# Performance work log

Measured on AMD Instinct MI355X. Metric: run time of the kernel, lower is better.

Reference implementation:

```python
import jax, jax.numpy as jnp
import numpy as np

# Llama-3.2-1B-style int4-quantized decoder (4 layers, reduced vocab)
L, D, H, HD, KVH, DFF, V, B, S = 4, 2048, 32, 64, 8, 8192, 32000, 4, 1024
ROPE_THETA = 500000.0


def setup_inputs() -> dict:
    key = jax.random.key(0)
    ks = jax.random.split(key, 18)
    def qw(k, shape):  # int4 weights stored in int32 carrier, range [-8, 8)
        return jax.random.randint(k, shape, -8, 8, dtype=jnp.int32)
    def sc(k, shape):  # per-output-channel dequant scales
        return jax.random.uniform(k, shape, jnp.float32, 0.005, 0.02)
    DKV = KVH * HD
    return {
        "token_ids": jax.random.randint(ks[0], (B, S), 0, V, dtype=jnp.int32),
        "embed": jax.random.normal(ks[1], (V, D), jnp.float32) * 0.02,
        "gamma_attn": jnp.ones((L, D), jnp.float32),
        "gamma_mlp": jnp.ones((L, D), jnp.float32),
        "gamma_final": jnp.ones((D,), jnp.float32),
        "wq": qw(ks[2], (L, D, D)),   "sq": sc(ks[3], (L, D)),
        "wk": qw(ks[4], (L, DKV, D)), "sk": sc(ks[5], (L, DKV)),
        "wv": qw(ks[6], (L, DKV, D)), "sv": sc(ks[7], (L, DKV)),
        "wo": qw(ks[8], (L, D, D)),   "so": sc(ks[9], (L, D)),
        "wg": qw(ks[10], (L, DFF, D)), "sg": sc(ks[11], (L, DFF)),
        "wu": qw(ks[12], (L, DFF, D)), "su": sc(ks[13], (L, DFF)),
        "wd": qw(ks[14], (L, D, DFF)), "sd": sc(ks[15], (L, D)),
    }


def _rmsnorm(x, g, eps=1e-5):
    return x * jax.lax.rsqrt(jnp.mean(x * x, axis=-1, keepdims=True) + eps) * g


def _rope(x):  # x: [B, S, n_heads, HD], split-half rotation (Llama convention)
    half = HD // 2
    inv_freq = ROPE_THETA ** (-jnp.arange(half, dtype=jnp.float32) * 2.0 / HD)
    ang = jnp.arange(x.shape[1], dtype=jnp.float32)[:, None] * inv_freq  # [S, half]
    cos = jnp.cos(ang)[None, :, None, :]
    sin = jnp.sin(ang)[None, :, None, :]
    x1, x2 = jnp.split(x, 2, axis=-1)
    return jnp.concatenate([x1 * cos - x2 * sin, x1 * sin + x2 * cos], axis=-1)


def _qlin(x, w_int, scale):
    # int4 dequant (per-out-channel symmetric) + matmul: y = x @ (w_int*scale)^T
    w = w_int.astype(jnp.float32) * scale[:, None]
    return jnp.einsum('bsd,od->bso', x, w)


def _forward(token_ids, embed, gamma_attn, gamma_mlp, gamma_final,
             wq, sq, wk, sk, wv, sv, wo, so, wg, sg, wu, su, wd, sd):
    x = embed[token_ids]                                    # [B, S, D]
    causal = jnp.tril(jnp.ones((S, S), dtype=bool))
    for l in range(L):
        # --- attention block ---
        h = _rmsnorm(x, gamma_attn[l])
        q = _qlin(h, wq[l], sq[l]).reshape(B, S, H, HD)
        k = _qlin(h, wk[l], sk[l]).reshape(B, S, KVH, HD)
        v = _qlin(h, wv[l], sv[l]).reshape(B, S, KVH, HD)
        q, k = _rope(q), _rope(k)
        k = jnp.repeat(k, H // KVH, axis=2)                 # GQA expand
        v = jnp.repeat(v, H // KVH, axis=2)
        scores = jnp.einsum('bqhd,bkhd->bhqk', q, k) / np.float32(np.sqrt(HD))
        scores = jnp.where(causal, scores, jnp.float32(-1e9))
        p = jax.nn.softmax(scores, axis=-1)
        attn = jnp.einsum('bhqk,bkhd->bqhd', p, v).reshape(B, S, D)
        x = x + _qlin(attn, wo[l], so[l])
        # --- SwiGLU MLP block ---
        h = _rmsnorm(x, gamma_mlp[l])
        g = jax.nn.silu(_qlin(h, wg[l], sg[l]))
        u = _qlin(h, wu[l], su[l])
        x = x + _qlin(g * u, wd[l], sd[l])
    x = _rmsnorm(x, gamma_final)
    # tied-embedding LM head; next-token logits at last position (decode step)
    return x[:, -1, :] @ embed.T                             # [B, V]


def reference(token_ids, embed, gamma_attn, gamma_mlp, gamma_final,
              wq, sq, wk, sk, wv, sv, wo, so, wg, sg, wu, su, wd, sd):
    return _forward(token_ids, embed, gamma_attn, gamma_mlp, gamma_final,
                    wq, sq, wk, sk, wv, sv, wo, so, wg, sg, wu, su, wd, sd)
```

## Files before the change

### kernel.cpp

```cpp
#include <hip/hip_runtime.h>
#include <hip/hip_bf16.h>

#define D_MODEL 2048
#define NH 32
#define HDIM 64
#define KVHEADS 8
#define DKV 512
#define DFF 8192
#define SEQ 1024
#define BATCH 4
#define NTOK 4096
#define VOCAB 32000
#define NLAYER 4

typedef __attribute__((ext_vector_type(8))) _Float16 f16x8;
typedef __attribute__((ext_vector_type(4))) _Float16 f16x4;
typedef __attribute__((ext_vector_type(4))) float f32x4;

static __device__ __forceinline__ void gload16(const void* g, void* l){
    __builtin_amdgcn_global_load_lds(
        (const __attribute__((address_space(1))) unsigned int*)g,
        (__attribute__((address_space(3))) unsigned int*)l, 16, 0, 0);
}

#define MFMA(d, x, y) d = __builtin_amdgcn_mfma_f32_16x16x32_f16(x, y, d, 0, 0, 0)
#define BAR()    __builtin_amdgcn_s_barrier()
#define LGK0()   do{ asm volatile("s_waitcnt lgkmcnt(0)" ::: "memory"); \
                     __builtin_amdgcn_sched_barrier(0); }while(0)
#define PRIO(x)  __builtin_amdgcn_s_setprio(x)

__global__ __launch_bounds__(256)
void gather_kernel(const int* __restrict__ tok, const float* __restrict__ embed,
                   float* __restrict__ X)
{
    int row = blockIdx.x;
    int id = tok[row];
    const float4* s = (const float4*)(embed + (size_t)id * D_MODEL);
    float4* d = (float4*)(X + (size_t)row * D_MODEL);
    d[threadIdx.x]       = s[threadIdx.x];
    d[threadIdx.x + 256] = s[threadIdx.x + 256];
}

__global__ __launch_bounds__(256)
void rope_table_kernel(float2* __restrict__ rt)
{
    int idx = blockIdx.x * 256 + threadIdx.x;
    int pos = idx >> 5, d = idx & 31;
    float inv = powf(500000.0f, -(float)d * (1.0f / 32.0f));
    float ang = (float)pos * inv;
    float s, c;
    sincosf(ang, &s, &c);
    rt[idx] = make_float2(c, s);
}

__global__ __launch_bounds__(256)
void wconv_all_kernel(const int* __restrict__ wq, const int* __restrict__ wk,
                      const int* __restrict__ wv, const int* __restrict__ wo,
                      const int* __restrict__ wg, const int* __restrict__ wu,
                      const int* __restrict__ wd, _Float16* __restrict__ O)
{
    int i = blockIdx.x * 256 + threadIdx.x;
    const int* s; int loc;
    if      (i <  1048576){ s = wq; loc = i; }
    else if (i <  1310720){ s = wk; loc = i - 1048576; }
    else if (i <  1572864){ s = wv; loc = i - 1310720; }
    else if (i <  2621440){ s = wo; loc = i - 1572864; }
    else if (i <  6815744){ s = wg; loc = i - 2621440; }
    else if (i < 11010048){ s = wu; loc = i - 6815744; }
    else                  { s = wd; loc = i - 11010048; }
    int4 w = ((const int4*)s)[loc];
    f16x4 o;
    o.x = (_Float16)(float)w.x; o.y = (_Float16)(float)w.y;
    o.z = (_Float16)(float)w.z; o.w = (_Float16)(float)w.w;
    ((f16x4*)O)[i] = o;
}

__global__ __launch_bounds__(256)
void rmsnorm_kernel(const float* __restrict__ X, const float* __restrict__ gamma,
                    _Float16* __restrict__ O)
{
    int row = blockIdx.x;
    const float* x = X + (size_t)row * D_MODEL;
    _Float16* o = O + (size_t)row * D_MODEL;
    int t = threadIdx.x;
    float4 v[2];
    float ss = 0.f;
#pragma unroll
    for (int i = 0; i < 2; i++){
        v[i] = *(const float4*)&x[(t + i*256)*4];
        ss += v[i].x*v[i].x + v[i].y*v[i].y + v[i].z*v[i].z + v[i].w*v[i].w;
    }
    for (int off = 32; off; off >>= 1) ss += __shfl_xor(ss, off, 64);
    __shared__ float red[4];
    __shared__ float invs;
    int lane = t & 63, wid = t >> 6;
    if (lane == 0) red[wid] = ss;
    __syncthreads();
    if (t == 0){
        float s = red[0] + red[1] + red[2] + red[3];
        invs = 1.0f / sqrtf(s / (float)D_MODEL + 1e-5f);
    }
    __syncthreads();
    float inv = invs;
#pragma unroll
    for (int i = 0; i < 2; i++){
        float4 g = *(const float4*)&gamma[(t + i*256)*4];
        f16x4 r;
        r.x = (_Float16)(v[i].x * inv * g.x); r.y = (_Float16)(v[i].y * inv * g.y);
        r.z = (_Float16)(v[i].z * inv * g.z); r.w = (_Float16)(v[i].w * inv * g.w);
        *(f16x4*)&o[(t + i*256)*4] = r;
    }
}

__global__ __launch_bounds__(256)
void final_norm_kernel(const float* __restrict__ X, const float* __restrict__ gamma,
                       float* __restrict__ XF)
{
    int b = blockIdx.x;
    const float* x = X + ((size_t)b * SEQ + SEQ - 1) * D_MODEL;
    float* o = XF + (size_t)b * D_MODEL;
    int t = threadIdx.x;
    float4 v[2];
    float ss = 0.f;
#pragma unroll
    for (int i = 0; i < 2; i++){
        v[i] = *(const float4*)&x[(t + i*256)*4];
        ss += v[i].x*v[i].x + v[i].y*v[i].y + v[i].z*v[i].z + v[i].w*v[i].w;
    }
    for (int off = 32; off; off >>= 1) ss += __shfl_xor(ss, off, 64);
    __shared__ float red[4];
    __shared__ float invs;
    int lane = t & 63, wid = t >> 6;
    if (lane == 0) red[wid] = ss;
    __syncthreads();
    if (t == 0){
        float s = red[0] + red[1] + red[2] + red[3];
        invs = 1.0f / sqrtf(s / (float)D_MODEL + 1e-5f);
    }
    __syncthreads();
    float inv = invs;
#pragma unroll
    for (int i = 0; i < 2; i++){
        float4 g = *(const float4*)&gamma[(t + i*256)*4];
        float4 r;
        r.x = v[i].x * inv * g.x; r.y = v[i].y * inv * g.y;
        r.z = v[i].z * inv * g.z; r.w = v[i].w * inv * g.w;
        *(float4*)&o[(t + i*256)*4] = r;
    }
}

__global__ __launch_bounds__(512, 2)
void gemm_mlp(const _Float16* __restrict__ A, const _Float16* __restrict__ WU,
              const _Float16* __restrict__ WG,
              const float* __restrict__ su, const float* __restrict__ sg,
              _Float16* __restrict__ U, int MT, int NT, int K)
{
    __shared__ __align__(16) _Float16 AS[2][256 * 64];
    __shared__ __align__(16) _Float16 US[2][128 * 64];
    __shared__ __align__(16) _Float16 GS[3][128 * 64];

    int nwg = MT * NT;
    int flat = blockIdx.x;
    int q = nwg >> 3, r = nwg & 7;
    int xcd = flat & 7, lid = flat >> 3;
    int swz = (xcd < r ? xcd * (q + 1) : r * (q + 1) + (xcd - r) * q) + lid;
    int bm = swz % MT, bn = swz / MT;
    int m0 = bm * 256, n0 = bn * 128;

    const int t = threadIdx.x;
    const int lane = t & 63, wid = t >> 6;
    const int ln15 = lane & 15, lq = lane >> 4;
    const int wm = wid >> 1, wn = wid & 1;
    const int sw = ln15 & 7;
    const int sl0 = (lq ^ sw) * 8, sl1 = ((4 + lq) ^ sw) * 8;

    const _Float16* srcA[4]; const _Float16* srcU[2]; const _Float16* srcG[2];
#pragma unroll
    for (int rr = 0; rr < 4; rr++){
        int ch = rr * 512 + t;
        int row = ch >> 3, s = (ch & 7) ^ (row & 7);
        srcA[rr] = A + (size_t)(m0 + row) * K + s * 8;
    }
#pragma unroll
    for (int rr = 0; rr < 2; rr++){
        int ch = rr * 512 + t;
        int row = ch >> 3, s = (ch & 7) ^ (row & 7);
        srcU[rr] = WU + (size_t)(n0 + row) * K + s * 8;
        srcG[rr] = WG + (size_t)(n0 + row) * K + s * 8;
    }
#define STG_A4(tile) do{ int _b = (tile) & 1; \
    gload16(srcA[0] + (size_t)(tile)*64, &AS[_b][(wid*64)*8]); \
    gload16(srcA[1] + (size_t)(tile)*64, &AS[_b][(512 + wid*64)*8]); \
    gload16(srcA[2] + (size_t)(tile)*64, &AS[_b][(1024 + wid*64)*8]); \
    gload16(srcA[3] + (size_t)(tile)*64, &AS[_b][(1536 + wid*64)*8]); }while(0)
#define STG_U2(tile) do{ int _b = (tile) & 1; \
    gload16(srcU[0] + (size_t)(tile)*64, &US[_b][(wid*64)*8]); \
    gload16(srcU[1] + (size_t)(tile)*64, &US[_b][(512 + wid*64)*8]); }while(0)
#define STG_G3(tile) do{ int _b = (tile) % 3; \
    gload16(srcG[0] + (size_t)(tile)*64, &GS[_b][(wid*64)*8]); \
    gload16(srcG[1] + (size_t)(tile)*64, &GS[_b][(512 + wid*64)*8]); }while(0)

    f32x4 accU[4][4], accG[4][4];
#pragma unroll
    for (int i = 0; i < 4; i++)
#pragma unroll
        for (int j = 0; j < 4; j++){
            accU[i][j] = (f32x4){0.f, 0.f, 0.f, 0.f};
            accG[i][j] = (f32x4){0.f, 0.f, 0.f, 0.f};
        }

    const int KT = K >> 6;

    STG_A4(0); STG_U2(0); STG_G3(0); STG_G3(1);
    asm volatile("s_waitcnt vmcnt(2)" ::: "memory");
    BAR();

    for (int kt = 0; kt < KT; ++kt){
        int cur = kt & 1, gcur = kt % 3;
        const _Float16* Ac = AS[cur];
        const _Float16* Uc = US[cur];
        const _Float16* Gc = GS[gcur];
        bool s1 = (kt + 1 < KT), s2 = (kt + 2 < KT);

        f16x8 afk0[4], afk1[4], buk0[4], buk1[4];
#pragma unroll
        for (int mf = 0; mf < 4; mf++)
            afk0[mf] = *(const f16x8*)&Ac[(wm * 64 + mf * 16 + ln15) * 64 + sl0];
#pragma unroll
        for (int nf = 0; nf < 4; nf++)
            buk0[nf] = *(const f16x8*)&Uc[(wn * 64 + nf * 16 + ln15) * 64 + sl0];
        if (s1) STG_A4(kt + 1);
        BAR(); LGK0(); PRIO(1);
#pragma unroll
        for (int mf = 0; mf < 4; mf++)
#pragma unroll
            for (int nf = 0; nf < 4; nf++)
                MFMA(accU[mf][nf], afk0[mf], buk0[nf]);
        PRIO(0); BAR();

#pragma unroll
        for (int mf = 0; mf < 4; mf++)
            afk1[mf] = *(const f16x8*)&Ac[(wm * 64 + mf * 16 + ln15) * 64 + sl1];
#pragma unroll
        for (int nf = 0; nf < 4; nf++)
            buk1[nf] = *(const f16x8*)&Uc[(wn * 64 + nf * 16 + ln15) * 64 + sl1];
        if (s1) STG_U2(kt + 1);
        BAR(); LGK0(); PRIO(1);
#pragma unroll
        for (int mf = 0; mf < 4; mf++)
#pragma unroll
            for (int nf = 0; nf < 4; nf++)
                MFMA(accU[mf][nf], afk1[mf], buk1[nf]);
        PRIO(0); BAR();

        f16x8 bgk0[4], bgk1[4];
#pragma unroll
        for (int nf = 0; nf < 4; nf++){
            bgk0[nf] = *(const f16x8*)&Gc[(wn * 64 + nf * 16 + ln15) * 64 + sl0];
            bgk1[nf] = *(const f16x8*)&Gc[(wn * 64 + nf * 16 + ln15) * 64 + sl1];
        }
        if (s2) STG_G3(kt + 2);
        BAR(); LGK0(); PRIO(1);
#pragma unroll
        for (int mf = 0; mf < 4; mf++)
#pragma unroll
            for (int nf = 0; nf < 4; nf++)
                MFMA(accG[mf][nf], afk0[mf], bgk0[nf]);
        PRIO(0); BAR();

        PRIO(1);
#pragma unroll
        for (int mf = 0; mf < 4; mf++)
#pragma unroll
            for (int nf = 0; nf < 4; nf++)
                MFMA(accG[mf][nf], afk1[mf], bgk1[nf]);
        PRIO(0);
        if (s1){
            if (s2) asm volatile("s_waitcnt vmcnt(2)" ::: "memory");
            else    asm volatile("s_waitcnt vmcnt(0)" ::: "memory");
            BAR();
            __builtin_amdgcn_sched_barrier(0);
        }
    }
#undef STG_A4
#undef STG_U2
#undef STG_G3

#pragma unroll
    for (int mf = 0; mf < 4; mf++){
        int rowb = m0 + wm * 64 + mf * 16 + lq * 4;
#pragma unroll
        for (int nf = 0; nf < 4; nf++){
            int colg = n0 + wn * 64 + nf * 16 + ln15;
            float scu = su[colg], scg = sg[colg];
#pragma unroll
            for (int rr2 = 0; rr2 < 4; rr2++){
                float uv = accU[mf][nf][rr2] * scu;
                float gv = accG[mf][nf][rr2] * scg;
                float sig = 1.0f / (1.0f + expf(-gv));
                U[(size_t)(rowb + rr2) * DFF + colg] = (_Float16)(gv * sig * uv);
            }
        }
    }
}

template<int EPI>
__global__ __launch_bounds__(512, 2)
void gemm_small(const _Float16* __restrict__ A, const _Float16* __restrict__ W,
                const float* __restrict__ sc0, const float* __restrict__ sc1,
                const float* __restrict__ sc2,
                void* __restrict__ C0, void* __restrict__ C1, void* __restrict__ C2,
                const float2* __restrict__ rt,
                int MT, int NT, int N, int K)
{
    __shared__ __align__(16) _Float16 AS[3][128 * 64];
    __shared__ __align__(16) _Float16 BS[3][256 * 64];

    int nwg = MT * NT;
    int flat = blockIdx.x;
    int q = nwg >> 3, r = nwg & 7;
    int xcd = flat & 7, lid = flat >> 3;
    int swz = (xcd < r ? xcd * (q + 1) : r * (q + 1) + (xcd - r) * q) + lid;
    int bm = swz % MT, bn = swz / MT;
    int m0 = bm * 128, n0 = bn * 256;

    const int t = threadIdx.x;
    const int lane = t & 63, wid = t >> 6;
    const int ln15 = lane & 15, lq = lane >> 4;
    const int wm = wid >> 2, wn = wid & 3;
    const int sw = ln15 & 7;
    const int sl0 = (lq ^ sw) * 8, sl1 = ((4 + lq) ^ sw) * 8;

    const _Float16* srcA[2]; const _Float16* srcB[4];
#pragma unroll
    for (int rr = 0; rr < 2; rr++){
        int ch = rr * 512 + t;
        int row = ch >> 3, s = (ch & 7) ^ (row & 7);
        srcA[rr] = A + (size_t)(m0 + row) * K + s * 8;
    }
#pragma unroll
    for (int rr = 0; rr < 4; rr++){
        int ch = rr * 512 + t;
        int row = ch >> 3, s = (ch & 7) ^ (row & 7);
        srcB[rr] = W + (size_t)(n0 + row) * K + s * 8;
    }
#define STG_A3(tile) do{ int _b = (tile) % 3; \
    gload16(srcA[0] + (size_t)(tile)*64, &AS[_b][(wid*64)*8]); \
    gload16(srcA[1] + (size_t)(tile)*64, &AS[_b][(512 + wid*64)*8]); }while(0)
#define STG_B3(tile) do{ int _b = (tile) % 3; \
    gload16(srcB[0] + (size_t)(tile)*64, &BS[_b][(wid*64)*8]); \
    gload16(srcB[1] + (size_t)(tile)*64, &BS[_b][(512 + wid*64)*8]); \
    gload16(srcB[2] + (size_t)(tile)*64, &BS[_b][(1024 + wid*64)*8]); \
    gload16(srcB[3] + (size_t)(tile)*64, &BS[_b][(1536 + wid*64)*8]); }while(0)

    f32x4 acc[4][4];
#pragma unroll
    for (int i = 0; i < 4; i++)
#pragma unroll
        for (int j = 0; j < 4; j++) acc[i][j] = (f32x4){0.f, 0.f, 0.f, 0.f};

    const int KT = K >> 6;

    STG_A3(0); STG_B3(0); STG_A3(1); STG_B3(1);
    asm volatile("s_waitcnt vmcnt(6)" ::: "memory");
    BAR();

    for (int kt = 0; kt < KT; ++kt){
        int cur = kt % 3;
        const _Float16* Ac = AS[cur];
        const _Float16* Bc = BS[cur];
        bool s1 = (kt + 1 < KT), s2 = (kt + 2 < KT);

        f16x8 af0[4], af1[4], bk0[4], bk1[4];
#pragma unroll
        for (int mf = 0; mf < 4; mf++)
            af0[mf] = *(const f16x8*)&Ac[(wm * 64 + mf * 16 + ln15) * 64 + sl0];
#pragma unroll
        for (int nf = 0; nf < 4; nf++)
            bk0[nf] = *(const f16x8*)&Bc[(wn * 64 + nf * 16 + ln15) * 64 + sl0];
        if (s2) STG_B3(kt + 2);
        BAR(); LGK0(); PRIO(1);
#pragma unroll
        for (int mf = 0; mf < 4; mf++)
#pragma unroll
            for (int nf = 0; nf < 4; nf++)
                MFMA(acc[mf][nf], af0[mf], bk0[nf]);
        PRIO(0); BAR();

#pragma unroll
        for (int mf = 0; mf < 4; mf++)
            af1[mf] = *(const f16x8*)&Ac[(wm * 64 + mf * 16 + ln15) * 64 + sl1];
#pragma unroll
        for (int nf = 0; nf < 4; nf++)
            bk1[nf] = *(const f16x8*)&Bc[(wn * 64 + nf * 16 + ln15) * 64 + sl1];
        if (s2) STG_A3(kt + 2);
        BAR(); LGK0(); PRIO(1);
#pragma unroll
        for (int mf = 0; mf < 4; mf++)
#pragma unroll
            for (int nf = 0; nf < 4; nf++)
                MFMA(acc[mf][nf], af1[mf], bk1[nf]);
        PRIO(0);
        if (s1){
            if (s2) asm volatile("s_waitcnt vmcnt(6)" ::: "memory");
            else    asm volatile("s_waitcnt vmcnt(0)" ::: "memory");
            BAR();
            __builtin_amdgcn_sched_barrier(0);
        }
    }
#undef STG_A3
#undef STG_B3

    if (EPI == 3){
        const float* sp; _Float16* dp; int nloc, nstr;
        if (n0 < 2048)      { sp = sc0; dp = (_Float16*)C0; nloc = n0;        nstr = 2048; }
        else if (n0 < 2560) { sp = sc1; dp = (_Float16*)C1; nloc = n0 - 2048; nstr = 512; }
        else                { sp = sc2; dp = (_Float16*)C2; nloc = n0 - 2560; nstr = 512; }
        bool dorope = (n0 < 2560);
        if (dorope){
#pragma unroll
            for (int mf = 0; mf < 4; mf++){
                int rowb = m0 + wm * 64 + mf * 16 + lq * 4;
#pragma unroll
                for (int nf = 0; nf < 2; nf++){
                    int colg = wn * 64 + nf * 16 + ln15;
                    int d = nf * 16 + ln15;
                    float s1v = sp[nloc + colg], s2v = sp[nloc + colg + 32];
#pragma unroll
                    for (int rr2 = 0; rr2 < 4; rr2++){
                        int row = rowb + rr2;
                        int pos = row & (SEQ - 1);
                        float2 cs = rt[pos * 32 + d];
                        float x1 = acc[mf][nf][rr2] * s1v;
                        float x2 = acc[mf][nf + 2][rr2] * s2v;
                        dp[(size_t)row * nstr + nloc + colg]      = (_Float16)(x1 * cs.x - x2 * cs.y);
                        dp[(size_t)row * nstr + nloc + colg + 32] = (_Float16)(x1 * cs.y + x2 * cs.x);
                    }
                }
            }
        } else {
#pragma unroll
            for (int mf = 0; mf < 4; mf++){
                int rowb = m0 + wm * 64 + mf * 16 + lq * 4;
#pragma unroll
                for (int nf = 0; nf < 4; nf++){
                    int colg = wn * 64 + nf * 16 + ln15;
                    float sc = sp[nloc + colg];
#pragma unroll
                    for (int rr2 = 0; rr2 < 4; rr2++)
                        dp[(size_t)(rowb + rr2) * nstr + nloc + colg] =
                            (_Float16)(acc[mf][nf][rr2] * sc);
                }
            }
        }
    } else {
#pragma unroll
        for (int mf = 0; mf < 4; mf++){
            int rowb = m0 + wm * 64 + mf * 16 + lq * 4;
#pragma unroll
            for (int nf = 0; nf < 4; nf++){
                int colg = n0 + wn * 64 + nf * 16 + ln15;
                float sc = sc0[colg];
#pragma unroll
                for (int rr2 = 0; rr2 < 4; rr2++){
                    size_t idx = (size_t)(rowb + rr2) * N + colg;
                    float val = acc[mf][nf][rr2] * sc;
                    if (EPI == 0){
                        ((_Float16*)C0)[idx] = (_Float16)val;
                    } else {
                        ((float*)C0)[idx] += val;
                    }
                }
            }
        }
    }
}

__global__ __launch_bounds__(256)
void attn_kernel(const _Float16* __restrict__ Qb, const _Float16* __restrict__ Kb,
                 const _Float16* __restrict__ Vb, _Float16* __restrict__ Ob)
{
    int bid = blockIdx.x;
    int qt = bid >> 7, h = bid & 31, b = (bid >> 5) & 3;
    int kvh = h >> 2;
    int q0 = qt * 128;
    int t = threadIdx.x, lane = t & 63, wid = t >> 6;
    int ln15 = lane & 15, lq = lane >> 4;

    __shared__ __align__(16) _Float16 Ksm[64 * 72];
    __shared__ __align__(16) _Float16 Vt[64 * 72];
    __shared__ __align__(16) _Float16 Pl[128 * 72];

    f16x8 qf[2][2];
    int qrow_g = b * SEQ + q0 + wid * 32;
#pragma unroll
    for (int mf = 0; mf < 2; mf++)
#pragma unroll
        for (int dc = 0; dc < 2; dc++)
            qf[mf][dc] = *(const f16x8*)(Qb + (size_t)(qrow_g + mf * 16 + ln15) * D_MODEL
                                         + h * HDIM + dc * 32 + lq * 8);

    f32x4 outv[2][4];
#pragma unroll
    for (int i = 0; i < 2; i++)
#pragma unroll
        for (int j = 0; j < 4; j++) outv[i][j] = (f32x4){0.f, 0.f, 0.f, 0.f};
    float mrun[2][4], lrun[2][4];
#pragma unroll
    for (int i = 0; i < 2; i++)
#pragma unroll
        for (int r = 0; r < 4; r++){ mrun[i][r] = -1e30f; lrun[i][r] = 0.f; }

    int ntile = (q0 + 128) >> 6;
    int ld_row = (t + 0) >> 3, ld_c8 = t & 7;
    int ld_row1 = (t + 256) >> 3;

    f16x8 k8[2], v8[2];
    {
        size_t base0 = (size_t)(b * SEQ + ld_row) * DKV + kvh * HDIM + ld_c8 * 8;
        size_t base1 = (size_t)(b * SEQ + ld_row1) * DKV + kvh * HDIM + ld_c8 * 8;
        k8[0] = *(const f16x8*)&Kb[base0];  v8[0] = *(const f16x8*)&Vb[base0];
        k8[1] = *(const f16x8*)&Kb[base1];  v8[1] = *(const f16x8*)&Vb[base1];
    }

    for (int kt = 0; kt < ntile; kt++){
        __syncthreads();
#pragma unroll
        for (int i = 0; i < 2; i++){
            int row = (i == 0) ? ld_row : ld_row1;
            *(f16x8*)&Ksm[row * 72 + ld_c8 * 8] = k8[i];
#pragma unroll
            for (int j = 0; j < 8; j++)
                Vt[(ld_c8 * 8 + j) * 72 + row] = v8[i][j];
        }
        __syncthreads();

        if (kt + 1 < ntile){
            size_t base0 = (size_t)(b * SEQ + (kt + 1) * 64 + ld_row) * DKV + kvh * HDIM + ld_c8 * 8;
            size_t base1 = (size_t)(b * SEQ + (kt + 1) * 64 + ld_row1) * DKV + kvh * HDIM + ld_c8 * 8;
            k8[0] = *(const f16x8*)&Kb[base0];  v8[0] = *(const f16x8*)&Vb[base0];
            k8[1] = *(const f16x8*)&Kb[base1];  v8[1] = *(const f16x8*)&Vb[base1];
        }

#pragma unroll
        for (int mf = 0; mf < 2; mf++){
            f32x4 sa[4];
#pragma unroll
            for (int kvf = 0; kvf < 4; kvf++) sa[kvf] = (f32x4){0.f, 0.f, 0.f, 0.f};
#pragma unroll
            for (int kvf = 0; kvf < 4; kvf++)
#pragma unroll
                for (int dc = 0; dc < 2; dc++){
                    f16x8 kb = *(const f16x8*)&Ksm[(kvf * 16 + ln15) * 72 + dc * 32 + lq * 8];
                    sa[kvf] = __builtin_amdgcn_mfma_f32_16x16x32_f16(qf[mf][dc], kb, sa[kvf], 0, 0, 0);
                }
            int qbase = q0 + wid * 32 + mf * 16 + lq * 4;
            float rowmax[4] = {-1e30f, -1e30f, -1e30f, -1e30f};
#pragma unroll
            for (int kvf = 0; kvf < 4; kvf++){
                int kva = kt * 64 + kvf * 16 + ln15;
#pragma unroll
                for (int r = 0; r < 4; r++){
                    float sv = sa[kvf][r] * 0.125f;
                    if (kva > qbase + r) sv = -1e9f;
                    sa[kvf][r] = sv;
                    rowmax[r] = fmaxf(rowmax[r], sv);
                }
            }
#pragma unroll
            for (int r = 0; r < 4; r++){
                rowmax[r] = fmaxf(rowmax[r], __shfl_xor(rowmax[r], 1, 64));
                rowmax[r] = fmaxf(rowmax[r], __shfl_xor(rowmax[r], 2, 64));
                rowmax[r] = fmaxf(rowmax[r], __shfl_xor(rowmax[r], 4, 64));
                rowmax[r] = fmaxf(rowmax[r], __shfl_xor(rowmax[r], 8, 64));
            }
            float scl[4], rsum[4];
#pragma unroll
            for (int r = 0; r < 4; r++){
                float mo = mrun[mf][r];
                float mn = fmaxf(mo, rowmax[r]);
                scl[r] = expf(mo - mn);
                mrun[mf][r] = mn;
                rsum[r] = 0.f;
            }
#pragma unroll
            for (int kvf = 0; kvf < 4; kvf++)
#pragma unroll
                for (int r = 0; r < 4; r++){
                    float p = expf(sa[kvf][r] - mrun[mf][r]);
                    sa[kvf][r] = p;
                    rsum[r] += p;
                }
#pragma unroll
            for (int r = 0; r < 4; r++){
                rsum[r] += __shfl_xor(rsum[r], 1, 64);
                rsum[r] += __shfl_xor(rsum[r], 2, 64);
                rsum[r] += __shfl_xor(rsum[r], 4, 64);
                rsum[r] += __shfl_xor(rsum[r], 8, 64);
                lrun[mf][r] = lrun[mf][r] * scl[r] + rsum[r];
            }
#pragma unroll
            for (int dfr = 0; dfr < 4; dfr++)
#pragma unroll
                for (int r = 0; r < 4; r++) outv[mf][dfr][r] *= scl[r];
#pragma unroll
            for (int kvf = 0; kvf < 4; kvf++)
#pragma unroll
                for (int r = 0; r < 4; r++)
                    Pl[(wid * 32 + mf * 16 + lq * 4 + r) * 72 + kvf * 16 + ln15] = (_Float16)sa[kvf][r];
        }
        __syncthreads();

#pragma unroll
        for (int mf = 0; mf < 2; mf++)
#pragma unroll
            for (int kc = 0; kc < 2; kc++){
                f16x8 pa = *(const f16x8*)&Pl[(wid * 32 + mf * 16 + ln15) * 72 + kc * 32 + lq * 8];
#pragma unroll
                for (int dfr = 0; dfr < 4; dfr++){
                    f16x8 vb = *(const f16x8*)&Vt[(dfr * 16 + ln15) * 72 + kc * 32 + lq * 8];
                    outv[mf][dfr] = __builtin_amdgcn_mfma_f32_16x16x32_f16(pa, vb, outv[mf][dfr], 0, 0, 0);
                }
            }
    }

#pragma unroll
    for (int mf = 0; mf < 2; mf++)
#pragma unroll
        for (int dfr = 0; dfr < 4; dfr++)
#pragma unroll
            for (int r = 0; r < 4; r++){
                float val = outv[mf][dfr][r] / lrun[mf][r];
                size_t row = (size_t)(b * SEQ + q0 + wid * 32 + mf * 16 + lq * 4 + r);
                Ob[row * D_MODEL + h * HDIM + dfr * 16 + ln15] = (_Float16)val;
            }
}

__global__ __launch_bounds__(256)
void lmhead_kernel(const float* __restrict__ XF, const float* __restrict__ embed,
                   float* __restrict__ out)
{
    __shared__ float xl[4 * D_MODEL];
    int t = threadIdx.x;
#pragma unroll
    for (int i = 0; i < 8; i++){
        int f = t + i * 256;
        ((float4*)xl)[f] = ((const float4*)XF)[f];
    }
    __syncthreads();
    int lane = t & 63, wid = t >> 6;
    for (int rr = 0; rr < 16; rr++){
        int vrow = blockIdx.x * 64 + wid * 16 + rr;
        const float4* er = (const float4*)(embed + (size_t)vrow * D_MODEL);
        float acc[4] = {0.f, 0.f, 0.f, 0.f};
        for (int j = 0; j < 8; j++){
            float4 e = er[lane + 64 * j];
#pragma unroll
            for (int b = 0; b < 4; b++){
                float4 xv = ((float4*)xl)[b * 512 + lane + 64 * j];
                acc[b] += e.x * xv.x + e.y * xv.y + e.z * xv.z + e.w * xv.w;
            }
        }
#pragma unroll
        for (int b = 0; b < 4; b++)
            for (int off = 32; off; off >>= 1) acc[b] += __shfl_xor(acc[b], off, 64);
        if (lane == 0){
#pragma unroll
            for (int b = 0; b < 4; b++)
                out[(size_t)b * VOCAB + vrow] = acc[b];
        }
    }
}

extern "C" void kernel_launch(void* const* d_in, const int* in_sizes, int n_in,
                              void* d_out, int out_size, void* d_ws, size_t ws_size,
                              hipStream_t stream)
{
    const int*   tok   = (const int*)d_in[0];
    const float* embed = (const float*)d_in[1];
    const float* g_attn = (const float*)d_in[2];
    const float* g_mlp  = (const float*)d_in[3];
    const float* g_fin  = (const float*)d_in[4];
    const int*   wq = (const int*)d_in[5];  const float* sq = (const float*)d_in[6];
    const int*   wk = (const int*)d_in[7];  const float* sk = (const float*)d_in[8];
    const int*   wv = (const int*)d_in[9];  const float* sv = (const float*)d_in[10];
    const int*   wo = (const int*)d_in[11]; const float* so = (const float*)d_in[12];
    const int*   wg = (const int*)d_in[13]; const float* sg = (const float*)d_in[14];
    const int*   wu = (const int*)d_in[15]; const float* su = (const float*)d_in[16];
    const int*   wd = (const int*)d_in[17]; const float* sd = (const float*)d_in[18];
    float* out = (float*)d_out;

    char* p = (char*)d_ws;
    _Float16* Wf = (_Float16*)p;  p += (size_t)60817408 * 2;
    float*    X  = (float*)p;     p += (size_t)NTOK * D_MODEL * 4;
    _Float16* Hb = (_Float16*)p;  p += (size_t)NTOK * D_MODEL * 2;
    _Float16* Qb = (_Float16*)p;  p += (size_t)NTOK * D_MODEL * 2;
    _Float16* Kb = (_Float16*)p;  p += (size_t)NTOK * DKV * 2;
    _Float16* Vb = (_Float16*)p;  p += (size_t)NTOK * DKV * 2;
    _Float16* Ab = (_Float16*)p;  p += (size_t)NTOK * D_MODEL * 2;
    _Float16* Ub = (_Float16*)p;  p += (size_t)NTOK * DFF * 2;
    float*    XF = (float*)p;     p += (size_t)BATCH * D_MODEL * 4;
    float2*   RT = (float2*)p;    p += (size_t)SEQ * 32 * 8;

    _Float16* wqf = Wf;
    _Float16* wkf = wqf + (size_t)D_MODEL * D_MODEL;
    _Float16* wvf = wkf + (size_t)DKV * D_MODEL;
    _Float16* wof = wvf + (size_t)DKV * D_MODEL;
    _Float16* wgf = wof + (size_t)D_MODEL * D_MODEL;
    _Float16* wuf = wgf + (size_t)DFF * D_MODEL;
    _Float16* wdf = wuf + (size_t)DFF * D_MODEL;

    gather_kernel<<<NTOK, 256, 0, stream>>>(tok, embed, X);
    rope_table_kernel<<<SEQ * 32 / 256, 256, 0, stream>>>(RT);

    for (int l = 0; l < NLAYER; l++){
        wconv_all_kernel<<<15204352 / 256, 256, 0, stream>>>(
            wq + (size_t)l * D_MODEL * D_MODEL,
            wk + (size_t)l * DKV * D_MODEL,
            wv + (size_t)l * DKV * D_MODEL,
            wo + (size_t)l * D_MODEL * D_MODEL,
            wg + (size_t)l * DFF * D_MODEL,
            wu + (size_t)l * DFF * D_MODEL,
            wd + (size_t)l * D_MODEL * DFF,
            Wf);

        rmsnorm_kernel<<<NTOK, 256, 0, stream>>>(X, g_attn + (size_t)l * D_MODEL, Hb);
        gemm_small<3><<<32 * 12, 512, 0, stream>>>(Hb, wqf,
            sq + (size_t)l * D_MODEL, sk + (size_t)l * DKV, sv + (size_t)l * DKV,
            Qb, Kb, Vb, RT, 32, 12, 3072, D_MODEL);
        attn_kernel<<<1024, 256, 0, stream>>>(Qb, Kb, Vb, Ab);
        gemm_small<1><<<32 * 8, 512, 0, stream>>>(Ab, wof,
            so + (size_t)l * D_MODEL, nullptr, nullptr,
            X, nullptr, nullptr, nullptr, 32, 8, D_MODEL, D_MODEL);

        rmsnorm_kernel<<<NTOK, 256, 0, stream>>>(X, g_mlp + (size_t)l * D_MODEL, Hb);
        gemm_mlp<<<16 * 64, 512, 0, stream>>>(Hb, wuf, wgf,
            su + (size_t)l * DFF, sg + (size_t)l * DFF, Ub, 16, 64, D_MODEL);
        gemm_small<1><<<32 * 8, 512, 0, stream>>>(Ub, wdf,
            sd + (size_t)l * D_MODEL, nullptr, nullptr,
            X, nullptr, nullptr, nullptr, 32, 8, D_MODEL, DFF);
    }

    final_norm_kernel<<<BATCH, 256, 0, stream>>>(X, g_fin, XF);
    lmhead_kernel<<<VOCAB / 64, 256, 0, stream>>>(XF, embed, out);
}
```

Measured before the change: 3.244 ms.

## Triple-buffer U weights and rebalance async load issue across MFMA phases

In the fused gate/up MLP GEMM, the U weight tile moves from double to triple buffering so U and G are both prefetched two tiles ahead. The A tile loads are split into two halves issued in separate compute phases, and the wait count is adjusted to match. In the generic GEMM, the A and B loads are regrouped into two balanced stages of three loads each instead of a 4/2 split. The goal is to spread global-to-LDS traffic evenly across MFMA phases. The extra LDS buffer raises shared memory use, so the launch bound drops from 2 blocks to 1 block per CU, which lowers occupancy.

```diff
diff --git a/kernel.cpp b/kernel.cpp
--- a/kernel.cpp
+++ b/kernel.cpp
@@ -149,14 +149,14 @@
     }
 }
 
-__global__ __launch_bounds__(512, 2)
+__global__ __launch_bounds__(512, 1)
 void gemm_mlp(const _Float16* __restrict__ A, const _Float16* __restrict__ WU,
               const _Float16* __restrict__ WG,
               const float* __restrict__ su, const float* __restrict__ sg,
               _Float16* __restrict__ U, int MT, int NT, int K)
 {
     __shared__ __align__(16) _Float16 AS[2][256 * 64];
-    __shared__ __align__(16) _Float16 US[2][128 * 64];
+    __shared__ __align__(16) _Float16 US[3][128 * 64];
     __shared__ __align__(16) _Float16 GS[3][128 * 64];
 
     int nwg = MT * NT;
@@ -188,15 +188,16 @@
         srcU[rr] = WU + (size_t)(n0 + row) * K + s * 8;
         srcG[rr] = WG + (size_t)(n0 + row) * K + s * 8;
     }
-#define STG_A4(tile) do{ int _b = (tile) & 1; \
+#define STG_A2a(tile) do{ int _b = (tile) & 1; \
     gload16(srcA[0] + (size_t)(tile)*64, &AS[_b][(wid*64)*8]); \
-    gload16(srcA[1] + (size_t)(tile)*64, &AS[_b][(512 + wid*64)*8]); \
+    gload16(srcA[1] + (size_t)(tile)*64, &AS[_b][(512 + wid*64)*8]); }while(0)
+#define STG_A2b(tile) do{ int _b = (tile) & 1; \
     gload16(srcA[2] + (size_t)(tile)*64, &AS[_b][(1024 + wid*64)*8]); \
     gload16(srcA[3] + (size_t)(tile)*64, &AS[_b][(1536 + wid*64)*8]); }while(0)
-#define STG_U2(tile) do{ int _b = (tile) & 1; \
+#define STG_U2(tile) do{ int _b = (tile) % 3; \
     gload16(srcU[0] + (size_t)(tile)*64, &US[_b][(wid*64)*8]); \
     gload16(srcU[1] + (size_t)(tile)*64, &US[_b][(512 + wid*64)*8]); }while(0)
-#define STG_G3(tile) do{ int _b = (tile) % 3; \
+#define STG_G2(tile) do{ int _b = (tile) % 3; \
     gload16(srcG[0] + (size_t)(tile)*64, &GS[_b][(wid*64)*8]); \
     gload16(srcG[1] + (size_t)(tile)*64, &GS[_b][(512 + wid*64)*8]); }while(0)
 
@@ -211,15 +212,16 @@
 
     const int KT = K >> 6;
 
-    STG_A4(0); STG_U2(0); STG_G3(0); STG_G3(1);
-    asm volatile("s_waitcnt vmcnt(2)" ::: "memory");
+    STG_A2a(0); STG_A2b(0); STG_U2(0); STG_G2(0);
+    STG_U2(1);  STG_G2(1);
+    asm volatile("s_waitcnt vmcnt(4)" ::: "memory");
     BAR();
 
     for (int kt = 0; kt < KT; ++kt){
-        int cur = kt & 1, gcur = kt % 3;
+        int cur = kt & 1, w3 = kt % 3;
         const _Float16* Ac = AS[cur];
-        const _Float16* Uc = US[cur];
-        const _Float16* Gc = GS[gcur];
+        const _Float16* Uc = US[w3];
+        const _Float16* Gc = GS[w3];
         bool s1 = (kt + 1 < KT), s2 = (kt + 2 < KT);
 
         f16x8 afk0[4], afk1[4], buk0[4], buk1[4];
@@ -229,7 +231,7 @@
 #pragma unroll
         for (int nf = 0; nf < 4; nf++)
             buk0[nf] = *(const f16x8*)&Uc[(wn * 64 + nf * 16 + ln15) * 64 + sl0];
-        if (s1) STG_A4(kt + 1);
+        if (s1) STG_A2a(kt + 1);
         BAR(); LGK0(); PRIO(1);
 #pragma unroll
         for (int mf = 0; mf < 4; mf++)
@@ -244,7 +246,7 @@
 #pragma unroll
         for (int nf = 0; nf < 4; nf++)
             buk1[nf] = *(const f16x8*)&Uc[(wn * 64 + nf * 16 + ln15) * 64 + sl1];
-        if (s1) STG_U2(kt + 1);
+        if (s1) STG_A2b(kt + 1);
         BAR(); LGK0(); PRIO(1);
 #pragma unroll
         for (int mf = 0; mf < 4; mf++)
@@ -259,7 +261,7 @@
             bgk0[nf] = *(const f16x8*)&Gc[(wn * 64 + nf * 16 + ln15) * 64 + sl0];
             bgk1[nf] = *(const f16x8*)&Gc[(wn * 64 + nf * 16 + ln15) * 64 + sl1];
         }
-        if (s2) STG_G3(kt + 2);
+        if (s2) STG_U2(kt + 2);
         BAR(); LGK0(); PRIO(1);
 #pragma unroll
         for (int mf = 0; mf < 4; mf++)
@@ -268,6 +270,7 @@
                 MFMA(accG[mf][nf], afk0[mf], bgk0[nf]);
         PRIO(0); BAR();
 
+        if (s2) STG_G2(kt + 2);
         PRIO(1);
 #pragma unroll
         for (int mf = 0; mf < 4; mf++)
@@ -276,15 +279,16 @@
                 MFMA(accG[mf][nf], afk1[mf], bgk1[nf]);
         PRIO(0);
         if (s1){
-            if (s2) asm volatile("s_waitcnt vmcnt(2)" ::: "memory");
+            if (s2) asm volatile("s_waitcnt vmcnt(4)" ::: "memory");
             else    asm volatile("s_waitcnt vmcnt(0)" ::: "memory");
             BAR();
             __builtin_amdgcn_sched_barrier(0);
         }
     }
-#undef STG_A4
+#undef STG_A2a
+#undef STG_A2b
 #undef STG_U2
-#undef STG_G3
+#undef STG_G2
 
 #pragma unroll
     for (int mf = 0; mf < 4; mf++){
@@ -344,14 +348,14 @@
         int row = ch >> 3, s = (ch & 7) ^ (row & 7);
         srcB[rr] = W + (size_t)(n0 + row) * K + s * 8;
     }
-#define STG_A3(tile) do{ int _b = (tile) % 3; \
-    gload16(srcA[0] + (size_t)(tile)*64, &AS[_b][(wid*64)*8]); \
-    gload16(srcA[1] + (size_t)(tile)*64, &AS[_b][(512 + wid*64)*8]); }while(0)
-#define STG_B3(tile) do{ int _b = (tile) % 3; \
+#define STG_P1(tile) do{ int _b = (tile) % 3; \
     gload16(srcB[0] + (size_t)(tile)*64, &BS[_b][(wid*64)*8]); \
     gload16(srcB[1] + (size_t)(tile)*64, &BS[_b][(512 + wid*64)*8]); \
+    gload16(srcA[0] + (size_t)(tile)*64, &AS[_b][(wid*64)*8]); }while(0)
+#define STG_P2(tile) do{ int _b = (tile) % 3; \
     gload16(srcB[2] + (size_t)(tile)*64, &BS[_b][(1024 + wid*64)*8]); \
-    gload16(srcB[3] + (size_t)(tile)*64, &BS[_b][(1536 + wid*64)*8]); }while(0)
+    gload16(srcB[3] + (size_t)(tile)*64, &BS[_b][(1536 + wid*64)*8]); \
+    gload16(srcA[1] + (size_t)(tile)*64, &AS[_b][(512 + wid*64)*8]); }while(0)
 
     f32x4 acc[4][4];
 #pragma unroll
@@ -361,7 +365,7 @@
 
     const int KT = K >> 6;
 
-    STG_A3(0); STG_B3(0); STG_A3(1); STG_B3(1);
+    STG_P1(0); STG_P2(0); STG_P1(1); STG_P2(1);
     asm volatile("s_waitcnt vmcnt(6)" ::: "memory");
     BAR();
 
@@ -378,7 +382,7 @@
 #pragma unroll
         for (int nf = 0; nf < 4; nf++)
             bk0[nf] = *(const f16x8*)&Bc[(wn * 64 + nf * 16 + ln15) * 64 + sl0];
-        if (s2) STG_B3(kt + 2);
+        if (s2) STG_P1(kt + 2);
         BAR(); LGK0(); PRIO(1);
 #pragma unroll
         for (int mf = 0; mf < 4; mf++)
@@ -393,7 +397,7 @@
 #pragma unroll
         for (int nf = 0; nf < 4; nf++)
             bk1[nf] = *(const f16x8*)&Bc[(wn * 64 + nf * 16 + ln15) * 64 + sl1];
-        if (s2) STG_A3(kt + 2);
+        if (s2) STG_P2(kt + 2);
         BAR(); LGK0(); PRIO(1);
 #pragma unroll
         for (int mf = 0; mf < 4; mf++)
@@ -408,8 +412,8 @@
             __builtin_amdgcn_sched_barrier(0);
         }
     }
-#undef STG_A3
-#undef STG_B3
+#undef STG_P1
+#undef STG_P2
 
     if (EPI == 3){
         const float* sp; _Float16* dp; int nloc, nstr;
```

After: 3.332 ms. 1.03x slower.
